# Optimization experiments

Hardware: AMD Instinct MI355X
Metric: run time of the kernel (lower is better)

## Reference

```python
import jax, jax.numpy as jnp
import numpy as np

B, T, C = 2, 1024, 256
DH = 8          # deformable head num
HD = 64         # head_dim
HN = C // HD    # head_num = 4


def grid_sample_bilinear(img, grid):
    """torch.nn.functional.grid_sample (bilinear, align_corners=True) for a
    single-channel image. img: (B,H,W); grid: (B,Ho,Wo,2) with grid[...,0]=x
    (width coord), grid[...,1]=y (height coord), both in [-1,1]."""
    B_, H, W = img.shape
    gx = (grid[..., 0] + 1.0) * 0.5 * (W - 1)
    gy = (grid[..., 1] + 1.0) * 0.5 * (H - 1)
    x0 = jnp.floor(gx)
    y0 = jnp.floor(gy)
    wx = gx - x0
    wy = gy - y0
    flat_img = img.reshape(B_, -1)

    def gather(iy, ix):
        iy = jnp.clip(iy.astype(jnp.int32), 0, H - 1)
        ix = jnp.clip(ix.astype(jnp.int32), 0, W - 1)
        flat = (iy * W + ix).reshape(B_, -1)
        return jnp.take_along_axis(flat_img, flat, axis=1).reshape(iy.shape)

    out = (gather(y0, x0) * (1 - wy) * (1 - wx)
           + gather(y0, x0 + 1) * (1 - wy) * wx
           + gather(y0 + 1, x0) * wy * (1 - wx)
           + gather(y0 + 1, x0 + 1) * wy * wx)
    return out  # (B, Ho, Wo)


def setup_inputs() -> dict:
    key = jax.random.key(0)
    ks = jax.random.split(key, 8)
    s = 1.0 / np.sqrt(C)
    return {
        "x": jax.random.normal(ks[0], (B, T, C), jnp.float32),
        "W_off1": jax.random.normal(ks[1], (C, C), jnp.float32) * s,
        "b_off1": jnp.zeros((C,), jnp.float32),
        "W_off2": jax.random.normal(ks[2], (C, DH * C * 2), jnp.float32) * s,
        "b_off2": jnp.zeros((DH * C * 2,), jnp.float32),
        "Wq": jax.random.normal(ks[3], (C, C), jnp.float32) * s,
        "bq": jnp.zeros((C,), jnp.float32),
        "Wk": jax.random.normal(ks[4], (C, C), jnp.float32) * s,
        "bk": jnp.zeros((C,), jnp.float32),
        "Wv": jax.random.normal(ks[5], (C, C), jnp.float32) * s,
        "bv": jnp.zeros((C,), jnp.float32),
        "Wo": jax.random.normal(ks[6], (DH * C, C), jnp.float32) / np.sqrt(DH * C),
        "bo": jnp.zeros((C,), jnp.float32),
    }


def reference(x, W_off1, b_off1, W_off2, b_off2, Wq, bq, Wk, bk, Wv, bv, Wo, bo):
    B_, T_, C_ = x.shape
    # offset network: per-token MLP -> DH heads of (C,2) grid coords in [-1,1]
    h = jax.nn.gelu(x @ W_off1 + b_off1)
    off = jnp.tanh((h @ W_off2 + b_off2).reshape(B_, T_, DH, C_, 2))
    off = off.transpose(0, 2, 1, 3, 4).reshape(B_, DH * T_, C_, 2)
    # deformable token resampling: x tiled DH times along token axis acts as
    # a 1-channel image of size (DH*T, C); grid_sample(bilinear, align_corners)
    img = jnp.tile(x, (1, DH, 1))                       # B x (DH*T) x C
    xs = grid_sample_bilinear(img, off)                 # B x (DH*T) x C
    xs = xs.reshape(B_ * DH, T_, C_)
    # multi-head attention over resampled tokens
    q = (xs @ Wq + bq).reshape(B_ * DH, T_, HN, HD)
    k = (xs @ Wk + bk).reshape(B_ * DH, T_, HN, HD)
    v = (xs @ Wv + bv).reshape(B_ * DH, T_, HN, HD)
    scores = jnp.einsum('bnhd,bkhd->bhnk', q, k) / np.float32(np.sqrt(HD))
    A = jax.nn.softmax(scores, axis=-1)
    out = jnp.einsum('bhnk,bkhd->bnhd', A, v).reshape(B_ * DH, T_, HN * HD)
    # gather deformable heads back and project
    out = out.reshape(B_, DH, T_, HN * HD).transpose(0, 2, 1, 3).reshape(B_, T_, DH * HN * HD)
    return out @ Wo + bo
```

## Files before the change

kernel.cpp:

```cpp
#include <hip/hip_runtime.h>
#include <hip/hip_bf16.h>

typedef __attribute__((ext_vector_type(8))) _Float16 half8;
typedef __attribute__((ext_vector_type(4))) _Float16 half4;
typedef __attribute__((ext_vector_type(4))) float f32x4;
typedef __attribute__((ext_vector_type(16))) float f32x16;
typedef __attribute__((ext_vector_type(2))) unsigned uint2v;
typedef __attribute__((ext_vector_type(4))) unsigned uint4v;

#define MFMAH(a, b, c) __builtin_amdgcn_mfma_f32_16x16x32_f16((a), (b), (c), 0, 0, 0)
#define MFMA32(a, b, c) __builtin_amdgcn_mfma_f32_32x32x16_f16((a), (b), (c), 0, 0, 0)

__device__ __forceinline__ short f2h(float v) { _Float16 h = (_Float16)v; return __builtin_bit_cast(short, h); }
__device__ __forceinline__ f32x4 fzero() { f32x4 z = {0.f, 0.f, 0.f, 0.f}; return z; }
__device__ __forceinline__ float u2f(unsigned u) { return __builtin_bit_cast(float, u); }
__device__ __forceinline__ unsigned f2u(float f) { return __builtin_bit_cast(unsigned, f); }

__device__ __forceinline__ void gl16(const void* g, void* l) {
    __builtin_amdgcn_global_load_lds((const __attribute__((address_space(1))) unsigned*)g,
                                     (__attribute__((address_space(3))) unsigned*)l, 16, 0, 0);
}

__device__ __forceinline__ float fast_tanh(float z) {
    float E = __expf(2.f * z);
    return 1.f - 2.f / (E + 1.f);
}

__device__ __forceinline__ float gelu_tanh(float v) {
    float u = 0.7978845608028654f * (v + 0.044715f * v * v * v);
    return 0.5f * v * (1.f + fast_tanh(u));
}


__global__ __launch_bounds__(256) void prep_all_k(
    const float* __restrict__ x, const float* __restrict__ Woff2,
    const float* __restrict__ Wq, const float* __restrict__ Wk, const float* __restrict__ Wv,
    const float* __restrict__ Wo,
    short* __restrict__ B2T, short* __restrict__ Wtqkv, short* __restrict__ WtoT,
    half4* __restrict__ Q)
{
    __shared__ float t[64][65];
    const int tid = threadIdx.x;
    const int bid = blockIdx.x;
    if (bid < 256) {
        const int bk = bid >> 6, bn = bid & 63;
        const int k0 = bk * 64, n0 = bn * 64;
#pragma unroll
        for (int p = 0; p < 16; ++p) {
            int idx = p * 256 + tid, r = idx >> 6, c = idx & 63;
            t[r][c] = Woff2[(long)(k0 + r) * 4096 + n0 + c];
        }
        __syncthreads();
#pragma unroll
        for (int p = 0; p < 16; ++p) {
            int idx = p * 256 + tid, nr = idx >> 6, kc = idx & 63;
            float v = t[kc][nr];
            _Float16 w1 = (_Float16)v;
            _Float16 w2 = (_Float16)(v - (float)w1);
            long base = (long)(n0 + nr) * 768 + k0 + kc;
            B2T[base]       = __builtin_bit_cast(short, w1);
            B2T[base + 256] = __builtin_bit_cast(short, w1);
            B2T[base + 512] = __builtin_bit_cast(short, w2);
        }
    } else if (bid < 1024) {
        int i = (bid - 256) * 256 + tid;
        int n = i >> 8, k = i & 255;
        const float* s = (n < 256) ? Wq : (n < 512) ? Wk : Wv;
        Wtqkv[i] = f2h(s[k * 256 + (n & 255)]);
    } else if (bid < 3072) {
        int i = (bid - 1024) * 256 + tid;
        int n = i >> 11, k = i & 2047;
        WtoT[i] = f2h(Wo[k * 256 + n]);
    } else {
        int i = (bid - 3072) * 256 + tid;
        int b = i >> 18, r = (i >> 8) & 1023, c = i & 255;
        const float* xb = x + (b << 18);
        int r1 = (r + 1) & 1023, c1 = (c + 1) & 255;
        half4 qv;
        qv[0] = (_Float16)xb[(r << 8) + c];
        qv[1] = (_Float16)xb[(r << 8) + c1];
        qv[2] = (_Float16)xb[(r1 << 8) + c];
        qv[3] = (_Float16)xb[(r1 << 8) + c1];
        Q[i] = qv;
    }
}


__global__ __launch_bounds__(256) void gemm1_k(const float* __restrict__ x, const float* __restrict__ W,
                                               const float* __restrict__ bias, short* __restrict__ hs) {
    __shared__ float As[64][17];
    __shared__ float Bs[16][68];
    const int tid = threadIdx.x;
    const int bm = blockIdx.x >> 2, bn = blockIdx.x & 3;
    const int m0 = bm * 64, n0 = bn * 64;
    const int ty = tid >> 4, tx = tid & 15;
    float acc[4][4] = {};
    const int ar = tid >> 2, ak = (tid & 3) << 2;
    const int bk = tid >> 4, bc = (tid & 15) << 2;

    for (int k0 = 0; k0 < 256; k0 += 16) {
        __syncthreads();
        float4 av = *(const float4*)(x + (m0 + ar) * 256 + k0 + ak);
        As[ar][ak + 0] = av.x; As[ar][ak + 1] = av.y; As[ar][ak + 2] = av.z; As[ar][ak + 3] = av.w;
        *(float4*)&Bs[bk][bc] = *(const float4*)(W + (k0 + bk) * 256 + n0 + bc);
        __syncthreads();
#pragma unroll
        for (int kk = 0; kk < 16; ++kk) {
            float a_[4], b_[4];
#pragma unroll
            for (int i = 0; i < 4; ++i) a_[i] = As[ty * 4 + i][kk];
            *(float4*)b_ = *(const float4*)&Bs[kk][tx * 4];
#pragma unroll
            for (int i = 0; i < 4; ++i)
#pragma unroll
                for (int j = 0; j < 4; ++j) acc[i][j] += a_[i] * b_[j];
        }
    }
#pragma unroll
    for (int i = 0; i < 4; ++i) {
        int row = m0 + ty * 4 + i;
#pragma unroll
        for (int j = 0; j < 4; ++j) {
            int col = n0 + tx * 4 + j;
            float v = gelu_tanh(acc[i][j] + bias[col]);
            _Float16 h1 = (_Float16)v;
            _Float16 h2 = (_Float16)(v - (float)h1);
            hs[row * 768 + col]       = __builtin_bit_cast(short, h1);
            hs[row * 768 + 256 + col] = __builtin_bit_cast(short, h2);
            hs[row * 768 + 512 + col] = __builtin_bit_cast(short, h1);
        }
    }
}


__global__ __launch_bounds__(256, 2) void gemm_samp(
    const short* __restrict__ A, const short* __restrict__ BT,
    const float* __restrict__ b0, short* __restrict__ out0, const half4* __restrict__ Q)
{
    __shared__ short lds[16384];
    short* As0 = lds;
    short* As1 = lds + 4096;
    short* Bs0 = lds + 8192;
    short* Bs1 = lds + 12288;

    const int tid = threadIdx.x;
    const int lane = tid & 63, w = tid >> 6;
    const int rl = lane & 15, g = lane >> 4;
    const int wr = w >> 1, wc = w & 1;
    const int bid = blockIdx.x;
    const int g2 = bid & 7, s = bid >> 3;
    const int bm = (g2 >> 2) * 8 + (s >> 3);
    const int bn = (g2 & 3) * 8 + (s & 7);
    const int m0 = bm << 7, n0 = bn << 7;

    f32x4 acc[4][4];
#pragma unroll
    for (int m = 0; m < 4; ++m)
#pragma unroll
        for (int n = 0; n < 4; ++n) acc[m][n] = fzero();

    const short* ap = A + (long)(m0 + w * 32 + (lane >> 2)) * 768 + ((lane & 3) << 3);
    const short* bp = BT + (long)(n0 + w * 32 + (lane >> 2)) * 768 + ((lane & 3) << 3);
    const int woff = w * 1024;

#define STAGE(dA, dB, kk) do { \
        gl16(ap + (kk), (dA) + woff); \
        gl16(ap + (kk) + 16 * 768, (dA) + woff + 512); \
        gl16(bp + (kk), (dB) + woff); \
        gl16(bp + (kk) + 16 * 768, (dB) + woff + 512); } while (0)

    STAGE(As0, Bs0, 0);
    for (int t = 0; t < 24; ++t) {
        const short* cA = (t & 1) ? As1 : As0;
        const short* cB = (t & 1) ? Bs1 : Bs0;
        short* nA = (t & 1) ? As0 : As1;
        short* nB = (t & 1) ? Bs0 : Bs1;
        if (t + 1 < 24) {
            STAGE(nA, nB, (t + 1) << 5);
            asm volatile("s_waitcnt vmcnt(4)" ::: "memory");
        } else {
            asm volatile("s_waitcnt vmcnt(0)" ::: "memory");
        }
        __builtin_amdgcn_s_barrier();
        half8 af[4], bf[4];
#pragma unroll
        for (int m = 0; m < 4; ++m) af[m] = *(const half8*)&cA[(wr * 64 + m * 16 + rl) * 32 + g * 8];
#pragma unroll
        for (int n = 0; n < 4; ++n) bf[n] = *(const half8*)&cB[(wc * 64 + n * 16 + rl) * 32 + g * 8];
#pragma unroll
        for (int m = 0; m < 4; ++m)
#pragma unroll
            for (int n = 0; n < 4; ++n) acc[m][n] = MFMAH(af[m], bf[n], acc[m][n]);
        __builtin_amdgcn_s_barrier();
    }
#undef STAGE

    const int jlo = (rl & 1) ? 2 : 0;
    float gxa[32], gya[32];
#pragma unroll
    for (int m = 0; m < 4; ++m)
#pragma unroll
        for (int nt = 0; nt < 4; ++nt) {
            const int col = n0 + wc * 64 + nt * 16 + rl;
            float o4[4], po4[4];
            const float bb = b0[col];
#pragma unroll
            for (int j = 0; j < 4; ++j) o4[j] = fast_tanh(acc[m][nt][j] + bb);
#pragma unroll
            for (int j = 0; j < 4; ++j) po4[j] = __shfl_xor(o4[j], 1);
#pragma unroll
            for (int u = 0; u < 2; ++u) {
                const int j = jlo + u;
                const int s2 = (m * 4 + nt) * 2 + u;
                gxa[s2] = (((rl & 1) ? po4[j] : o4[j]) + 1.f) * 127.5f;
                gya[s2] = (((rl & 1) ? o4[j] : po4[j]) + 1.f) * 4095.5f;
            }
        }
    half4 qv[32];
#pragma unroll
    for (int s2 = 0; s2 < 32; ++s2) {
        const int m = s2 >> 3, u = s2 & 1;
        const int rowl = wr * 64 + m * 16 + g * 4 + jlo + u;
        const int b = (m0 + rowl) >> 10;
        const int iy0 = (int)gya[s2], ix0 = (int)gxa[s2];
        qv[s2] = Q[((long)b << 18) + ((iy0 & 1023) << 8) + ix0];
    }
#pragma unroll
    for (int s2 = 0; s2 < 32; ++s2) {
        const int m = s2 >> 3, nt = (s2 >> 1) & 3, u = s2 & 1;
        const int rowl = wr * 64 + m * 16 + g * 4 + jlo + u;
        const int cl = (wc * 64 + nt * 16 + rl) >> 1;
        float gx = gxa[s2], gy = gya[s2];
        float wx = gx - floorf(gx), wy = gy - floorf(gy);
        float r = (float)qv[s2][0] * (1.f - wy) * (1.f - wx) + (float)qv[s2][1] * (1.f - wy) * wx
                + (float)qv[s2][2] * wy * (1.f - wx) + (float)qv[s2][3] * wy * wx;
        lds[rowl * 72 + cl] = f2h(r);
    }
    __syncthreads();
    const int d = n0 >> 9, c0 = (n0 >> 1) & 255;
    const int b = m0 >> 10, t0 = m0 & 1023;
    short* xo = out0 + ((long)(b * 8 + d) * 1024 + t0) * 256 + c0;
#pragma unroll
    for (int p = 0; p < 4; ++p) {
        int idx = p * 256 + tid, rowl = idx >> 3, ch = idx & 7;
        *(half8*)(xo + rowl * 256 + ch * 8) = *(const half8*)&lds[rowl * 72 + ch * 8];
    }
}


template <int EPI>
__global__ __launch_bounds__(256, 3) void gemm128(
    const short* __restrict__ A, const short* __restrict__ BT,
    const float* __restrict__ b0, const float* __restrict__ b1, const float* __restrict__ b2,
    void* __restrict__ out0, void* __restrict__ out1, void* __restrict__ out2,
    int M, int N, int K, int lda, int ldb)
{
    __shared__ short lds[16384];
    short* As0 = lds;
    short* As1 = lds + 4096;
    short* Bs0 = lds + 8192;
    short* Bs1 = lds + 12288;

    const int tid = threadIdx.x;
    const int lane = tid & 63, w = tid >> 6;
    const int rl = lane & 15, g = lane >> 4;
    const int wr = w >> 1, wc = w & 1;
    const int bid = blockIdx.x;
    int bm, bn;
    if (EPI == 2) {
        int s = bid >> 3;
        bm = (bid & 7) * 16 + s / 6;
        bn = s - (s / 6) * 6;
    } else {
        const int nb = N >> 7;
        bm = bid / nb;
        bn = bid % nb;
    }
    const int m0 = bm << 7, n0 = bn << 7;

    if (EPI == 3) { A += blockIdx.y << 8; BT += blockIdx.y << 8; }

    f32x4 acc[4][4];
#pragma unroll
    for (int m = 0; m < 4; ++m)
#pragma unroll
        for (int n = 0; n < 4; ++n) acc[m][n] = fzero();

    const short* ap = A + (long)(m0 + w * 32 + (lane >> 2)) * lda + ((lane & 3) << 3);
    const short* bp = BT + (long)(n0 + w * 32 + (lane >> 2)) * ldb + ((lane & 3) << 3);
    const int woff = w * 1024;

#define STAGE(dA, dB, kk) do { \
        gl16(ap + (kk), (dA) + woff); \
        gl16(ap + (kk) + 16 * lda, (dA) + woff + 512); \
        gl16(bp + (kk), (dB) + woff); \
        gl16(bp + (kk) + 16 * ldb, (dB) + woff + 512); } while (0)

    const int nt_ = K >> 5;
    STAGE(As0, Bs0, 0);
    for (int t = 0; t < nt_; ++t) {
        const short* cA = (t & 1) ? As1 : As0;
        const short* cB = (t & 1) ? Bs1 : Bs0;
        short* nA = (t & 1) ? As0 : As1;
        short* nB = (t & 1) ? Bs0 : Bs1;
        if (t + 1 < nt_) {
            STAGE(nA, nB, (t + 1) << 5);
            asm volatile("s_waitcnt vmcnt(4)" ::: "memory");
        } else {
            asm volatile("s_waitcnt vmcnt(0)" ::: "memory");
        }
        __builtin_amdgcn_s_barrier();
        half8 af[4], bf[4];
#pragma unroll
        for (int m = 0; m < 4; ++m) af[m] = *(const half8*)&cA[(wr * 64 + m * 16 + rl) * 32 + g * 8];
#pragma unroll
        for (int n = 0; n < 4; ++n) bf[n] = *(const half8*)&cB[(wc * 64 + n * 16 + rl) * 32 + g * 8];
#pragma unroll
        for (int m = 0; m < 4; ++m)
#pragma unroll
            for (int n = 0; n < 4; ++n) acc[m][n] = MFMAH(af[m], bf[n], acc[m][n]);
        __builtin_amdgcn_s_barrier();
    }
#undef STAGE

    if (EPI == 2) {
#pragma unroll
        for (int m = 0; m < 4; ++m)
#pragma unroll
            for (int nt = 0; nt < 4; ++nt) {
                const int cl = wc * 64 + nt * 16 + rl;
                const int col = n0 + cl;
#pragma unroll
                for (int j = 0; j < 4; ++j) {
                    const int tl = wr * 64 + m * 16 + g * 4 + j;
                    float v;
                    int slot;
                    if (bn < 2) {
                        v = (acc[m][nt][j] + b0[col]) * 0.18033688011112042f;
                        slot = tl * 128 + cl;
                    } else if (bn < 4) {
                        v = acc[m][nt][j] + b1[(bn - 2) * 128 + cl];
                        int hl = cl >> 6, dd = cl & 63;
                        int c = dd >> 4, hi2 = (dd >> 3) & 1, e = dd & 7;
                        int kkl = tl >> 5, l31t = tl & 31;
                        slot = (hl * 4 + kkl) * 2048 + (c * 64 + hi2 * 32 + l31t) * 8 + e;
                    } else {
                        v = acc[m][nt][j] + b2[(bn - 4) * 128 + cl];
                        int hl = cl >> 6, d = cl & 63;
                        int kkl = tl >> 5, chi = (tl >> 4) & 1, hi2 = (tl >> 3) & 1, e = tl & 7;
                        int c = chi * 2 + (d >> 5);
                        slot = (hl * 4 + kkl) * 2048 + (c * 64 + hi2 * 32 + (d & 31)) * 8 + e;
                    }
                    lds[slot] = f2h(v);
                }
            }
        __syncthreads();
        const int bh = m0 >> 10;
        if (bn < 2) {
            short* qo = (short*)out0 + (long)m0 * 256 + n0;
#pragma unroll
            for (int p = 0; p < 8; ++p) {
                int idx = p * 256 + tid, rowl = idx >> 4, ch = idx & 15;
                *(half8*)(qo + rowl * 256 + ch * 8) = *(const half8*)&lds[rowl * 128 + ch * 8];
            }
        } else {
            short* dst = (bn < 4) ? (short*)out1 : (short*)out2;
            const int hb = (bn < 4) ? (bn - 2) * 2 : (bn - 4) * 2;
            const int kk0 = (m0 & 1023) >> 5;
#pragma unroll
            for (int p = 0; p < 8; ++p) {
                int idx = p * 256 + tid, til = idx >> 8, wit = idx & 255;
                int hl = til >> 2, kkl = til & 3;
                long base = (((long)(bh * 4 + hb + hl) * 32) + kk0 + kkl) * 2048;
                *(half8*)(dst + base + wit * 8) = *(const half8*)&lds[til * 2048 + wit * 8];
            }
        }
    } else {
        float* op = (float*)out0 + (long)blockIdx.y * M * N;
#pragma unroll
        for (int m = 0; m < 4; ++m)
#pragma unroll
            for (int nt = 0; nt < 4; ++nt) {
                const int col = n0 + wc * 64 + nt * 16 + rl;
#pragma unroll
                for (int j = 0; j < 4; ++j) {
                    const long grow = m0 + wr * 64 + m * 16 + g * 4 + j;
                    op[grow * N + col] = acc[m][nt][j];
                }
            }
    }
}

__global__ void reduce_out_k(const float* __restrict__ p, const float* __restrict__ bo,
                             float* __restrict__ out) {
    int i = blockIdx.x * 256 + threadIdx.x;
    float s = bo[i & 255];
#pragma unroll
    for (int ks = 0; ks < 8; ++ks) s += p[ks * 524288 + i];
    out[i] = s;
}


__global__ __launch_bounds__(256) void attn_k(const short* __restrict__ q, const short* __restrict__ kc,
                                              const short* __restrict__ vc, short* __restrict__ oc) {
    __shared__ short kv[8192];
    const int tid = threadIdx.x;
    const int lane = tid & 63, w = tid >> 6;
    const int l31 = lane & 31, hi = lane >> 5;
    const int bhh = blockIdx.x & 63;
    const int bh = bhh >> 2, h = bhh & 3;
    const int q0 = (blockIdx.x >> 6) * 128 + w * 32;

    const short* qb = q + (long)bh * 262144 + h * 64;
    const short* kt = kc + (long)bhh * 65536;
    const short* vt = vc + (long)bhh * 65536;

    half8 qf[4];
#pragma unroll
    for (int c = 0; c < 4; ++c)
        qf[c] = *(const half8*)(qb + (long)(q0 + l31) * 256 + c * 16 + hi * 8);

    float m_ = -1e30f, l_ = 0.f;
    f32x16 O0, O1;
#pragma unroll
    for (int r = 0; r < 16; ++r) { O0[r] = 0.f; O1[r] = 0.f; }

    const int sw = w * 512 + lane * 8;

#define KVSTAGE(kk, b) do { \
        gl16(kt + (kk) * 2048 + sw, &kv[(b) * 4096 + w * 512]); \
        gl16(vt + (kk) * 2048 + sw, &kv[(b) * 4096 + 2048 + w * 512]); } while (0)

    KVSTAGE(0, 0);
    __syncthreads();
    for (int kk = 0; kk < 32; ++kk) {
        const int b = kk & 1;
        if (kk + 1 < 32) KVSTAGE(kk + 1, b ^ 1);
        half8 KD[4], VD[4];
#pragma unroll
        for (int c = 0; c < 4; ++c) {
            KD[c] = *(const half8*)&kv[b * 4096 + c * 512 + lane * 8];
            VD[c] = *(const half8*)&kv[b * 4096 + 2048 + c * 512 + lane * 8];
        }
        f32x16 S;
#pragma unroll
        for (int r = 0; r < 16; ++r) S[r] = 0.f;
#pragma unroll
        for (int c = 0; c < 4; ++c) S = MFMA32(KD[c], qf[c], S);
        float t8[8];
#pragma unroll
        for (int r = 0; r < 8; ++r) t8[r] = fmaxf(S[2 * r], S[2 * r + 1]);
        float mx = fmaxf(fmaxf(fmaxf(t8[0], t8[1]), fmaxf(t8[2], t8[3])),
                         fmaxf(fmaxf(t8[4], t8[5]), fmaxf(t8[6], t8[7])));
        uint2v sp = __builtin_amdgcn_permlane32_swap(f2u(mx), f2u(mx), false, false);
        mx = fmaxf(u2f(sp[0]), u2f(sp[1]));
        if (__any(mx > m_ + 8.f)) {
            float mn = fmaxf(m_, mx);
            float sc = exp2f(m_ - mn);
            m_ = mn;
            l_ *= sc;
#pragma unroll
            for (int r = 0; r < 16; ++r) { O0[r] *= sc; O1[r] *= sc; }
        }
        float p[16];
#pragma unroll
        for (int r = 0; r < 16; ++r) p[r] = exp2f(S[r] - m_);
        float s8[8];
#pragma unroll
        for (int r = 0; r < 8; ++r) s8[r] = p[2 * r] + p[2 * r + 1];
        float rs = (((s8[0] + s8[1]) + (s8[2] + s8[3])) + ((s8[4] + s8[5]) + (s8[6] + s8[7])));
        uint2v sq = __builtin_amdgcn_permlane32_swap(f2u(rs), f2u(rs), false, false);
        rs = u2f(sq[0]) + u2f(sq[1]);
        l_ += rs;
        half8 PA[2];
#pragma unroll
        for (int c = 0; c < 2; ++c) {
            const int o = c * 8;
            unsigned a0 = f2u(__builtin_bit_cast(float, __builtin_amdgcn_cvt_pkrtz(p[o + 0], p[o + 1])));
            unsigned b0v = f2u(__builtin_bit_cast(float, __builtin_amdgcn_cvt_pkrtz(p[o + 4], p[o + 5])));
            unsigned a1 = f2u(__builtin_bit_cast(float, __builtin_amdgcn_cvt_pkrtz(p[o + 2], p[o + 3])));
            unsigned b1v = f2u(__builtin_bit_cast(float, __builtin_amdgcn_cvt_pkrtz(p[o + 6], p[o + 7])));
            uint2v r0 = __builtin_amdgcn_permlane32_swap(a0, b0v, false, false);
            uint2v r1 = __builtin_amdgcn_permlane32_swap(a1, b1v, false, false);
            uint4v wpk = {r0[0], r1[0], r0[1], r1[1]};
            PA[c] = __builtin_bit_cast(half8, wpk);
        }
        O0 = MFMA32(VD[0], PA[0], O0);
        O1 = MFMA32(VD[1], PA[0], O1);
        O0 = MFMA32(VD[2], PA[1], O0);
        O1 = MFMA32(VD[3], PA[1], O1);
        __syncthreads();
    }
#undef KVSTAGE

    const float inv = 1.f / l_;
    const int b = bh >> 3, d = bh & 7;
    const int t = q0 + l31;
    short* ob = oc + ((long)(b * 1024 + t) * 8 + d) * 256 + h * 64;
#pragma unroll
    for (int rr = 0; rr < 8; ++rr) {
        int dvb = (rr & 1) * 2 + 8 * (rr >> 1) + 4 * hi;
        unsigned u0 = (unsigned short)f2h(O0[2 * rr] * inv) | ((unsigned)(unsigned short)f2h(O0[2 * rr + 1] * inv) << 16);
        unsigned u1 = (unsigned short)f2h(O1[2 * rr] * inv) | ((unsigned)(unsigned short)f2h(O1[2 * rr + 1] * inv) << 16);
        *(unsigned*)(ob + dvb) = u0;
        *(unsigned*)(ob + 32 + dvb) = u1;
    }
}


extern "C" void kernel_launch(void* const* d_in, const int* in_sizes, int n_in,
                              void* d_out, int out_size, void* d_ws, size_t ws_size,
                              hipStream_t stream) {
    const float* x     = (const float*)d_in[0];
    const float* Woff1 = (const float*)d_in[1];
    const float* boff1 = (const float*)d_in[2];
    const float* Woff2 = (const float*)d_in[3];
    const float* boff2 = (const float*)d_in[4];
    const float* Wq    = (const float*)d_in[5];
    const float* bq    = (const float*)d_in[6];
    const float* Wk    = (const float*)d_in[7];
    const float* bk    = (const float*)d_in[8];
    const float* Wv    = (const float*)d_in[9];
    const float* bv    = (const float*)d_in[10];
    const float* Wo    = (const float*)d_in[11];
    const float* bo    = (const float*)d_in[12];

    char* ws = (char*)d_ws;
    short* hsplit = (short*)(ws + 0);
    short* B2T    = (short*)(ws + 3145728);
    short* cat    = (short*)(ws + 0);
    short* Wtqkv  = (short*)(ws + 9437184);
    short* WtoT   = (short*)(ws + 9830400);
    short* xs     = (short*)(ws + 10878976);
    short* qbuf   = (short*)(ws + 19267584);
    short* kcoal  = (short*)(ws + 27656192);
    short* vcoal  = (short*)(ws + 36044800);
    half4* Qt     = (half4*)(ws + 44433408);
    float* parts  = (float*)(ws + 44433408);

    prep_all_k<<<5120, 256, 0, stream>>>(x, Woff2, Wq, Wk, Wv, Wo, B2T, Wtqkv, WtoT, Qt);

    gemm1_k<<<128, 256, 0, stream>>>(x, Woff1, boff1, hsplit);

    gemm_samp<<<512, 256, 0, stream>>>(hsplit, B2T, boff2, xs, Qt);

    gemm128<2><<<(16384 / 128) * (768 / 128), 256, 0, stream>>>(
        xs, Wtqkv, bq, bk, bv, qbuf, kcoal, vcoal, 16384, 768, 256, 256, 256);

    attn_k<<<512, 256, 0, stream>>>(qbuf, kcoal, vcoal, cat);

    gemm128<3><<<dim3((2048 / 128) * (256 / 128), 8), 256, 0, stream>>>(
        cat, WtoT, nullptr, nullptr, nullptr, parts, nullptr, nullptr, 2048, 256, 256, 2048, 2048);
    reduce_out_k<<<2048, 256, 0, stream>>>(parts, bo, (float*)d_out);
}
```

Baseline: 140.4 us.

## Halve gemm_samp N-tile to 64 and fuse sampling epilogue to raise occupancy

The offset GEMM with fused grid-sample now uses 128x64 tiles instead of 128x128, doubling the grid to 1024 blocks. LDS drops to 24KB and launch bounds allow 4 blocks per CU. The epilogue no longer buffers 32 coordinates and 32 gathered texels in registers; it computes, gathers and writes each sample inline, which lowers register pressure. The cost is more redundant A-tile loads across blocks and less latency hiding for the gathers, since they are no longer batched.

```diff
diff --git a/kernel.cpp b/kernel.cpp
--- a/kernel.cpp
+++ b/kernel.cpp
@@ -133,15 +133,15 @@
 }
 
 
-__global__ __launch_bounds__(256, 2) void gemm_samp(
+__global__ __launch_bounds__(256, 4) void gemm_samp(
     const short* __restrict__ A, const short* __restrict__ BT,
     const float* __restrict__ b0, short* __restrict__ out0, const half4* __restrict__ Q)
 {
-    __shared__ short lds[16384];
+    __shared__ short lds[12288];
     short* As0 = lds;
     short* As1 = lds + 4096;
     short* Bs0 = lds + 8192;
-    short* Bs1 = lds + 12288;
+    short* Bs1 = lds + 10240;
 
     const int tid = threadIdx.x;
     const int lane = tid & 63, w = tid >> 6;
@@ -149,25 +149,23 @@
     const int wr = w >> 1, wc = w & 1;
     const int bid = blockIdx.x;
     const int g2 = bid & 7, s = bid >> 3;
-    const int bm = (g2 >> 2) * 8 + (s >> 3);
-    const int bn = (g2 & 3) * 8 + (s & 7);
-    const int m0 = bm << 7, n0 = bn << 7;
-
-    f32x4 acc[4][4];
+    const int bm = (g2 >> 2) * 8 + (g2 & 3) * 2 + (s >> 6);
+    const int bn = s & 63;
+    const int m0 = bm << 7, n0 = bn << 6;
+
+    f32x4 acc[4][2];
 #pragma unroll
     for (int m = 0; m < 4; ++m)
 #pragma unroll
-        for (int n = 0; n < 4; ++n) acc[m][n] = fzero();
+        for (int n = 0; n < 2; ++n) acc[m][n] = fzero();
 
     const short* ap = A + (long)(m0 + w * 32 + (lane >> 2)) * 768 + ((lane & 3) << 3);
-    const short* bp = BT + (long)(n0 + w * 32 + (lane >> 2)) * 768 + ((lane & 3) << 3);
-    const int woff = w * 1024;
+    const short* bp = BT + (long)(n0 + w * 16 + (lane >> 2)) * 768 + ((lane & 3) << 3);
 
 #define STAGE(dA, dB, kk) do { \
-        gl16(ap + (kk), (dA) + woff); \
-        gl16(ap + (kk) + 16 * 768, (dA) + woff + 512); \
-        gl16(bp + (kk), (dB) + woff); \
-        gl16(bp + (kk) + 16 * 768, (dB) + woff + 512); } while (0)
+        gl16(ap + (kk), (dA) + w * 1024); \
+        gl16(ap + (kk) + 16 * 768, (dA) + w * 1024 + 512); \
+        gl16(bp + (kk), (dB) + w * 512); } while (0)
 
     STAGE(As0, Bs0, 0);
     for (int t = 0; t < 24; ++t) {
@@ -177,73 +175,61 @@
         short* nB = (t & 1) ? Bs0 : Bs1;
         if (t + 1 < 24) {
             STAGE(nA, nB, (t + 1) << 5);
-            asm volatile("s_waitcnt vmcnt(4)" ::: "memory");
+            asm volatile("s_waitcnt vmcnt(3)" ::: "memory");
         } else {
             asm volatile("s_waitcnt vmcnt(0)" ::: "memory");
         }
         __builtin_amdgcn_s_barrier();
-        half8 af[4], bf[4];
+        half8 af[4], bf[2];
 #pragma unroll
         for (int m = 0; m < 4; ++m) af[m] = *(const half8*)&cA[(wr * 64 + m * 16 + rl) * 32 + g * 8];
 #pragma unroll
-        for (int n = 0; n < 4; ++n) bf[n] = *(const half8*)&cB[(wc * 64 + n * 16 + rl) * 32 + g * 8];
+        for (int n = 0; n < 2; ++n) bf[n] = *(const half8*)&cB[(wc * 32 + n * 16 + rl) * 32 + g * 8];
 #pragma unroll
         for (int m = 0; m < 4; ++m)
 #pragma unroll
-            for (int n = 0; n < 4; ++n) acc[m][n] = MFMAH(af[m], bf[n], acc[m][n]);
+            for (int n = 0; n < 2; ++n) acc[m][n] = MFMAH(af[m], bf[n], acc[m][n]);
         __builtin_amdgcn_s_barrier();
     }
 #undef STAGE
 
     const int jlo = (rl & 1) ? 2 : 0;
-    float gxa[32], gya[32];
+    const int b = m0 >> 10;
 #pragma unroll
     for (int m = 0; m < 4; ++m)
 #pragma unroll
-        for (int nt = 0; nt < 4; ++nt) {
-            const int col = n0 + wc * 64 + nt * 16 + rl;
+        for (int nt = 0; nt < 2; ++nt) {
+            const int col = n0 + wc * 32 + nt * 16 + rl;
             float o4[4], po4[4];
             const float bb = b0[col];
 #pragma unroll
             for (int j = 0; j < 4; ++j) o4[j] = fast_tanh(acc[m][nt][j] + bb);
 #pragma unroll
             for (int j = 0; j < 4; ++j) po4[j] = __shfl_xor(o4[j], 1);
+            const int cl = (wc * 32 + nt * 16 + rl) >> 1;
 #pragma unroll
             for (int u = 0; u < 2; ++u) {
                 const int j = jlo + u;
-                const int s2 = (m * 4 + nt) * 2 + u;
-                gxa[s2] = (((rl & 1) ? po4[j] : o4[j]) + 1.f) * 127.5f;
-                gya[s2] = (((rl & 1) ? o4[j] : po4[j]) + 1.f) * 4095.5f;
+                float gx = (((rl & 1) ? po4[j] : o4[j]) + 1.f) * 127.5f;
+                float gy = (((rl & 1) ? o4[j] : po4[j]) + 1.f) * 4095.5f;
+                float x0f = floorf(gx), y0f = floorf(gy);
+                float wx = gx - x0f, wy = gy - y0f;
+                int ix0 = (int)x0f, iy0 = (int)y0f;
+                const int rowl = wr * 64 + m * 16 + g * 4 + j;
+                half4 qv = Q[((long)b << 18) + ((iy0 & 1023) << 8) + ix0];
+                float r = (float)qv[0] * (1.f - wy) * (1.f - wx) + (float)qv[1] * (1.f - wy) * wx
+                        + (float)qv[2] * wy * (1.f - wx) + (float)qv[3] * wy * wx;
+                lds[rowl * 36 + cl] = f2h(r);
             }
         }
-    half4 qv[32];
-#pragma unroll
-    for (int s2 = 0; s2 < 32; ++s2) {
-        const int m = s2 >> 3, u = s2 & 1;
-        const int rowl = wr * 64 + m * 16 + g * 4 + jlo + u;
-        const int b = (m0 + rowl) >> 10;
-        const int iy0 = (int)gya[s2], ix0 = (int)gxa[s2];
-        qv[s2] = Q[((long)b << 18) + ((iy0 & 1023) << 8) + ix0];
-    }
-#pragma unroll
-    for (int s2 = 0; s2 < 32; ++s2) {
-        const int m = s2 >> 3, nt = (s2 >> 1) & 3, u = s2 & 1;
-        const int rowl = wr * 64 + m * 16 + g * 4 + jlo + u;
-        const int cl = (wc * 64 + nt * 16 + rl) >> 1;
-        float gx = gxa[s2], gy = gya[s2];
-        float wx = gx - floorf(gx), wy = gy - floorf(gy);
-        float r = (float)qv[s2][0] * (1.f - wy) * (1.f - wx) + (float)qv[s2][1] * (1.f - wy) * wx
-                + (float)qv[s2][2] * wy * (1.f - wx) + (float)qv[s2][3] * wy * wx;
-        lds[rowl * 72 + cl] = f2h(r);
-    }
     __syncthreads();
     const int d = n0 >> 9, c0 = (n0 >> 1) & 255;
-    const int b = m0 >> 10, t0 = m0 & 1023;
+    const int t0 = m0 & 1023;
     short* xo = out0 + ((long)(b * 8 + d) * 1024 + t0) * 256 + c0;
 #pragma unroll
-    for (int p = 0; p < 4; ++p) {
-        int idx = p * 256 + tid, rowl = idx >> 3, ch = idx & 7;
-        *(half8*)(xo + rowl * 256 + ch * 8) = *(const half8*)&lds[rowl * 72 + ch * 8];
+    for (int p = 0; p < 2; ++p) {
+        int idx = p * 256 + tid, rowl = idx >> 2, ch = idx & 3;
+        *(half8*)(xo + rowl * 256 + ch * 8) = *(const half8*)&lds[rowl * 36 + ch * 8];
     }
 }
 
@@ -542,7 +528,7 @@
 
     gemm1_k<<<128, 256, 0, stream>>>(x, Woff1, boff1, hsplit);
 
-    gemm_samp<<<512, 256, 0, stream>>>(hsplit, B2T, boff2, xs, Qt);
+    gemm_samp<<<1024, 256, 0, stream>>>(hsplit, B2T, boff2, xs, Qt);
 
     gemm128<2><<<(16384 / 128) * (768 / 128), 256, 0, stream>>>(
         xs, Wtqkv, bq, bk, bv, qbuf, kcoal, vcoal, 16384, 768, 256, 256, 256);
```

New measurement: 147.6 us. 5.1% more time.

## Triple-buffer attention KV loads and fuse sampling epilogue to cut registers

Applied to the files above, without the earlier changes.

The attention kernel moves from double to triple buffering of K/V tiles in LDS. It issues loads two steps ahead, uses explicit vmcnt waits, and needs only one barrier per iteration instead of two, so global-load latency is better hidden. The sampling GEMM epilogue now computes grid coordinates, gathers and interpolates inline rather than holding 32-entry coordinate and gather arrays, and launch bounds rise from 2 to 3 waves to improve occupancy. The inline gather serializes load latency per sample, since the earlier code batched all loads before use, and attention LDS use grows by half.

```diff
diff --git a/kernel.cpp b/kernel.cpp
--- a/kernel.cpp
+++ b/kernel.cpp
@@ -133,7 +133,7 @@
 }
 
 
-__global__ __launch_bounds__(256, 2) void gemm_samp(
+__global__ __launch_bounds__(256, 3) void gemm_samp(
     const short* __restrict__ A, const short* __restrict__ BT,
     const float* __restrict__ b0, short* __restrict__ out0, const half4* __restrict__ Q)
 {
@@ -196,7 +196,6 @@
 #undef STAGE
 
     const int jlo = (rl & 1) ? 2 : 0;
-    float gxa[32], gya[32];
 #pragma unroll
     for (int m = 0; m < 4; ++m)
 #pragma unroll
@@ -208,34 +207,23 @@
             for (int j = 0; j < 4; ++j) o4[j] = fast_tanh(acc[m][nt][j] + bb);
 #pragma unroll
             for (int j = 0; j < 4; ++j) po4[j] = __shfl_xor(o4[j], 1);
+            const int cl = (wc * 64 + nt * 16 + rl) >> 1;
 #pragma unroll
             for (int u = 0; u < 2; ++u) {
                 const int j = jlo + u;
-                const int s2 = (m * 4 + nt) * 2 + u;
-                gxa[s2] = (((rl & 1) ? po4[j] : o4[j]) + 1.f) * 127.5f;
-                gya[s2] = (((rl & 1) ? o4[j] : po4[j]) + 1.f) * 4095.5f;
+                float gx = (((rl & 1) ? po4[j] : o4[j]) + 1.f) * 127.5f;
+                float gy = (((rl & 1) ? o4[j] : po4[j]) + 1.f) * 4095.5f;
+                float x0f = floorf(gx), y0f = floorf(gy);
+                float wx = gx - x0f, wy = gy - y0f;
+                int ix0 = (int)x0f, iy0 = (int)y0f;
+                const int rowl = wr * 64 + m * 16 + g * 4 + j;
+                const int b = (m0 + rowl) >> 10;
+                half4 qv = Q[((long)b << 18) + ((iy0 & 1023) << 8) + ix0];
+                float r = (float)qv[0] * (1.f - wy) * (1.f - wx) + (float)qv[1] * (1.f - wy) * wx
+                        + (float)qv[2] * wy * (1.f - wx) + (float)qv[3] * wy * wx;
+                lds[rowl * 72 + cl] = f2h(r);
             }
         }
-    half4 qv[32];
-#pragma unroll
-    for (int s2 = 0; s2 < 32; ++s2) {
-        const int m = s2 >> 3, u = s2 & 1;
-        const int rowl = wr * 64 + m * 16 + g * 4 + jlo + u;
-        const int b = (m0 + rowl) >> 10;
-        const int iy0 = (int)gya[s2], ix0 = (int)gxa[s2];
-        qv[s2] = Q[((long)b << 18) + ((iy0 & 1023) << 8) + ix0];
-    }
-#pragma unroll
-    for (int s2 = 0; s2 < 32; ++s2) {
-        const int m = s2 >> 3, nt = (s2 >> 1) & 3, u = s2 & 1;
-        const int rowl = wr * 64 + m * 16 + g * 4 + jlo + u;
-        const int cl = (wc * 64 + nt * 16 + rl) >> 1;
-        float gx = gxa[s2], gy = gya[s2];
-        float wx = gx - floorf(gx), wy = gy - floorf(gy);
-        float r = (float)qv[s2][0] * (1.f - wy) * (1.f - wx) + (float)qv[s2][1] * (1.f - wy) * wx
-                + (float)qv[s2][2] * wy * (1.f - wx) + (float)qv[s2][3] * wy * wx;
-        lds[rowl * 72 + cl] = f2h(r);
-    }
     __syncthreads();
     const int d = n0 >> 9, c0 = (n0 >> 1) & 255;
     const int b = m0 >> 10, t0 = m0 & 1023;
@@ -403,7 +391,7 @@
 
 __global__ __launch_bounds__(256) void attn_k(const short* __restrict__ q, const short* __restrict__ kc,
                                               const short* __restrict__ vc, short* __restrict__ oc) {
-    __shared__ short kv[8192];
+    __shared__ short kv[12288];
     const int tid = threadIdx.x;
     const int lane = tid & 63, w = tid >> 6;
     const int l31 = lane & 31, hi = lane >> 5;
@@ -432,15 +420,22 @@
         gl16(vt + (kk) * 2048 + sw, &kv[(b) * 4096 + 2048 + w * 512]); } while (0)
 
     KVSTAGE(0, 0);
-    __syncthreads();
+    KVSTAGE(1, 1);
+    int bc = 0, bs = 2;
     for (int kk = 0; kk < 32; ++kk) {
-        const int b = kk & 1;
-        if (kk + 1 < 32) KVSTAGE(kk + 1, b ^ 1);
+        if (kk < 31) asm volatile("s_waitcnt vmcnt(2)" ::: "memory");
+        else         asm volatile("s_waitcnt vmcnt(0)" ::: "memory");
+        __builtin_amdgcn_s_barrier();
+        if (kk + 2 < 32) {
+            KVSTAGE(kk + 2, bs);
+            bs = (bs == 2) ? 0 : bs + 1;
+        }
+        const int bb = bc * 4096;
         half8 KD[4], VD[4];
 #pragma unroll
         for (int c = 0; c < 4; ++c) {
-            KD[c] = *(const half8*)&kv[b * 4096 + c * 512 + lane * 8];
-            VD[c] = *(const half8*)&kv[b * 4096 + 2048 + c * 512 + lane * 8];
+            KD[c] = *(const half8*)&kv[bb + c * 512 + lane * 8];
+            VD[c] = *(const half8*)&kv[bb + 2048 + c * 512 + lane * 8];
         }
         f32x16 S;
 #pragma unroll
@@ -489,7 +484,7 @@
         O1 = MFMA32(VD[1], PA[0], O1);
         O0 = MFMA32(VD[2], PA[1], O0);
         O1 = MFMA32(VD[3], PA[1], O1);
-        __syncthreads();
+        bc = (bc == 2) ? 0 : bc + 1;
     }
 #undef KVSTAGE
 
```

Result: faster. 136.9 us (-2.5%).
